# Performance work log

Hardware: AMD Instinct MI355X
Metric: run time of the kernel (lower is better)

Reference implementation:

```python
import jax, jax.numpy as jnp
import numpy as np

B, S, D, H = 2, 2048, 1024, 16
DK = D // H
EPS = 1e-6  # torch RMSNorm default eps=None -> eps = finfo.eps? torch uses eps=None meaning torch.finfo(dtype).eps; use 1.1920929e-07
RMS_EPS = 1.1920929e-07


def setup_inputs() -> dict:
    key = jax.random.key(0)
    ks = jax.random.split(key, 10)
    std = 1.0 / np.sqrt(D)
    inp = {
        "x": jax.random.normal(ks[0], (B, S, D), jnp.float32),
        "mask": jnp.tril(jnp.ones((S, S), jnp.int32))[None, None],  # causal [1,1,S,S]
        "wq": jax.random.uniform(ks[1], (D, D), jnp.float32, -std, std),
        "bq": jax.random.uniform(ks[2], (D,), jnp.float32, -std, std),
        "wk": jax.random.uniform(ks[3], (D, D), jnp.float32, -std, std),
        "bk": jax.random.uniform(ks[4], (D,), jnp.float32, -std, std),
        "wv": jax.random.uniform(ks[5], (D, D), jnp.float32, -std, std),
        "bv": jax.random.uniform(ks[6], (D,), jnp.float32, -std, std),
        "wo": jax.random.uniform(ks[7], (D, D), jnp.float32, -std, std),
        "bo": jax.random.uniform(ks[8], (D,), jnp.float32, -std, std),
        "g": jnp.ones((D,), jnp.float32),  # RMSNorm weight
    }
    return inp


def reference(x, mask, wq, bq, wk, bk, wv, bv, wo, bo, g):
    # pre-RMSNorm
    ms = jnp.mean(x * x, axis=-1, keepdims=True)
    normed = x * jax.lax.rsqrt(ms + RMS_EPS) * g
    # QKV projections (torch Linear: y = x @ W^T + b), split into heads [B,H,S,DK]
    def proj(w, b):
        y = jnp.einsum('bsd,ed->bse', normed, w) + b
        return y.reshape(B, S, H, DK).transpose(0, 2, 1, 3)
    Q, K, V = proj(wq, bq), proj(wk, bk), proj(wv, bv)
    scores = jnp.einsum('bhqd,bhkd->bhqk', Q, K) / jnp.sqrt(jnp.float32(DK))
    scores = jnp.where(mask == 0, jnp.float32(-1e9), scores)
    attn = jax.nn.softmax(scores, axis=-1)
    ctx = jnp.einsum('bhqk,bhkd->bhqd', attn, V)
    ctx = ctx.transpose(0, 2, 1, 3).reshape(B, S, D)
    out = jnp.einsum('bsd,ed->bse', ctx, wo) + bo
    return x + out, attn
```

## Files before the change

### kernel.cpp

```cpp
#include <hip/hip_runtime.h>


typedef unsigned short u16;
typedef __attribute__((ext_vector_type(8))) short bf8_t;
typedef __attribute__((ext_vector_type(4))) float f4_t;

#define S_LEN 2048
#define NHEAD 16
#define RMS_EPS 1.1920929e-07f

__device__ inline u16 f2bf(float f) {
  union { float f; unsigned int i; } v; v.f = f;
  unsigned int r = v.i + 0x7fffu + ((v.i >> 16) & 1u);
  return (u16)(r >> 16);
}

__device__ inline void gll16(const void* g, void* l) {
  __builtin_amdgcn_global_load_lds(
      (const __attribute__((address_space(1))) void*)g,
      (__attribute__((address_space(3))) void*)l, 16, 0, 0);
}

__global__ __launch_bounds__(256) void prep_k(
    const float* __restrict__ wq, const float* __restrict__ wk,
    const float* __restrict__ wv, const float* __restrict__ wo,
    const float* __restrict__ bq, const float* __restrict__ bk,
    const float* __restrict__ bv, u16* __restrict__ Wcat,
    u16* __restrict__ Wob, float* __restrict__ bcat) {
  int idx = blockIdx.x * 256 + threadIdx.x;
  if (idx < 786432) {
    int z = idx / 262144, r = idx - z * 262144;
    const float* s = z == 0 ? wq : z == 1 ? wk : wv;
    float4 v = ((const float4*)s)[r];
    ((ushort4*)Wcat)[idx] =
        make_ushort4(f2bf(v.x), f2bf(v.y), f2bf(v.z), f2bf(v.w));
  } else if (idx < 786432 + 262144) {
    int r = idx - 786432;
    float4 v = ((const float4*)wo)[r];
    ((ushort4*)Wob)[r] = make_ushort4(f2bf(v.x), f2bf(v.y), f2bf(v.z), f2bf(v.w));
  } else if (idx < 786432 + 262144 + 768) {
    int r = idx - (786432 + 262144);
    int z = r >> 8, rr = r & 255;
    const float* s = z == 0 ? bq : z == 1 ? bk : bv;
    ((float4*)bcat)[r] = ((const float4*)s)[rr];
  }
}

__global__ __launch_bounds__(256) void rmsnorm_k(const float* __restrict__ x,
                                                 const float* __restrict__ g,
                                                 u16* __restrict__ out) {
  int row = blockIdx.x, tid = threadIdx.x;
  float4 v = ((const float4*)(x + (size_t)row * 1024))[tid];
  float ss = v.x * v.x + v.y * v.y + v.z * v.z + v.w * v.w;
#pragma unroll
  for (int o = 32; o > 0; o >>= 1) ss += __shfl_xor(ss, o);
  __shared__ float red[4];
  int wid = tid >> 6, lane = tid & 63;
  if (lane == 0) red[wid] = ss;
  __syncthreads();
  float rs = rsqrtf((red[0] + red[1] + red[2] + red[3]) * (1.0f / 1024.0f) +
                    RMS_EPS);
  float4 gv = ((const float4*)g)[tid];
  ((ushort4*)(out + (size_t)row * 1024))[tid] =
      make_ushort4(f2bf(v.x * rs * gv.x), f2bf(v.y * rs * gv.y),
                   f2bf(v.z * rs * gv.z), f2bf(v.w * rs * gv.w));
}

template <int MODE>
__global__ __launch_bounds__(256, 2) void gemm_mfma(
    const u16* __restrict__ A, const u16* __restrict__ Bm,
    const float* __restrict__ bias, const float* __restrict__ resid,
    u16* __restrict__ Oq, u16* __restrict__ Ok, u16* __restrict__ Ov,
    float* __restrict__ out1) {
  __shared__ u16 As[128 * 64];
  __shared__ u16 Bs[128 * 64];
  const int m0 = blockIdx.y * 128, n0 = blockIdx.x * 128;
  const int tid = threadIdx.x, l = tid & 63, w = tid >> 6;
  const int wr = w >> 1, wc = w & 1, lg = l >> 4, lo = l & 15;
  const int arow = tid >> 3;
  const int acol = (tid & 7) * 8;

  f4_t acc[4][4];
#pragma unroll
  for (int i = 0; i < 4; i++)
#pragma unroll
    for (int j = 0; j < 4; j++) acc[i][j] = {0.f, 0.f, 0.f, 0.f};

  for (int k0 = 0; k0 < 1024; k0 += 64) {
#pragma unroll
    for (int r = 0; r < 4; r++) {
      gll16(A + (size_t)(m0 + r * 32 + arow) * 1024 + k0 + acol,
            (char*)As + r * 4096 + w * 1024);
      gll16(Bm + (size_t)(n0 + r * 32 + arow) * 1024 + k0 + acol,
            (char*)Bs + r * 4096 + w * 1024);
    }
    __syncthreads();
#pragma unroll
    for (int ks = 0; ks < 2; ks++) {
      bf8_t af[4], bf[4];
#pragma unroll
      for (int mi = 0; mi < 4; mi++)
        af[mi] = *(const bf8_t*)(As + (wr * 64 + mi * 16 + lo) * 64 + ks * 32 +
                                 lg * 8);
#pragma unroll
      for (int ni = 0; ni < 4; ni++)
        bf[ni] = *(const bf8_t*)(Bs + (wc * 64 + ni * 16 + lo) * 64 + ks * 32 +
                                 lg * 8);
#pragma unroll
      for (int mi = 0; mi < 4; mi++)
#pragma unroll
        for (int ni = 0; ni < 4; ni++)
          acc[mi][ni] = __builtin_amdgcn_mfma_f32_16x16x32_bf16(
              af[mi], bf[ni], acc[mi][ni], 0, 0, 0);
    }
    __syncthreads();
  }

  if (MODE == 0) {
    const int z = n0 >> 10;
    u16* ob = z == 0 ? Oq : z == 1 ? Ok : Ov;
#pragma unroll
    for (int mi = 0; mi < 4; mi++)
#pragma unroll
      for (int ni = 0; ni < 4; ni++)
#pragma unroll
        for (int j = 0; j < 4; j++) {
          int m = m0 + wr * 64 + mi * 16 + lg * 4 + j;
          int n = n0 + wc * 64 + ni * 16 + lo;
          int nn = n & 1023, h = nn >> 6, d = nn & 63;
          int b = m >> 11, s = m & 2047;
          u16 vv = f2bf(acc[mi][ni][j] + bias[n]);
          if (z < 2)
            ob[(((size_t)(b * 16 + h) * 2048 + s) << 6) + d] = vv;
          else
            ob[((size_t)(b * 16 + h) * 64 + d) * 2048 + s] = vv;
        }
  } else {
#pragma unroll
    for (int mi = 0; mi < 4; mi++)
#pragma unroll
      for (int ni = 0; ni < 4; ni++)
#pragma unroll
        for (int j = 0; j < 4; j++) {
          int m = m0 + wr * 64 + mi * 16 + lg * 4 + j;
          int n = n0 + wc * 64 + ni * 16 + lo;
          out1[(size_t)m * 1024 + n] =
              acc[mi][ni][j] + bias[n] + resid[(size_t)m * 1024 + n];
        }
  }
}

__global__ __launch_bounds__(256, 2) void attn_k(
    const u16* __restrict__ Qb, const u16* __restrict__ Kb,
    const u16* __restrict__ Vt, float* __restrict__ attn,
    u16* __restrict__ ctx) {
  const int qt = blockIdx.x, bh = blockIdx.y;
  const int tid = threadIdx.x, l = tid & 63, w = tid >> 6;
  const int wr = w >> 1, wc = w & 1, lg = l >> 4, lo = l & 15;
  const int q0 = qt * 128, nkt = qt + 1;

  __shared__ u16 Pl[128 * 136];
  __shared__ u16 Vs[64 * 136];
  __shared__ float mred[2][128], lred[2][128];

  const u16* Qp = Qb + (size_t)bh * (2048 * 64);
  const u16* Kp = Kb + (size_t)bh * (2048 * 64);
  const u16* Vp = Vt + (size_t)bh * (64 * 2048);
  float* Ap = attn + (size_t)bh * ((size_t)2048 * 2048);

  {
    const int c0 = nkt * 128, cols4 = (2048 - c0) >> 2;
    float4 z4 = make_float4(0.f, 0.f, 0.f, 0.f);
    for (int r = 0; r < 128; r++) {
      float4* rp = (float4*)(Ap + (size_t)(q0 + r) * 2048 + c0);
      for (int c = tid; c < cols4; c += 256) rp[c] = z4;
    }
  }

  bf8_t qf[4][2];
#pragma unroll
  for (int mi = 0; mi < 4; mi++)
#pragma unroll
    for (int ks = 0; ks < 2; ks++)
      qf[mi][ks] = *(const bf8_t*)(Qp +
                                   (size_t)(q0 + wr * 64 + mi * 16 + lo) * 64 +
                                   ks * 32 + lg * 8);

  float rm[4][4], rl[4][4];
#pragma unroll
  for (int mi = 0; mi < 4; mi++)
#pragma unroll
    for (int j = 0; j < 4; j++) { rm[mi][j] = -3.0e38f; rl[mi][j] = 0.f; }

  for (int kt = 0; kt < nkt; kt++) {
    const int k0 = kt * 128;
    f4_t sa[4][4];
#pragma unroll
    for (int i = 0; i < 4; i++)
#pragma unroll
      for (int j = 0; j < 4; j++) sa[i][j] = {0.f, 0.f, 0.f, 0.f};
#pragma unroll
    for (int ks = 0; ks < 2; ks++) {
      bf8_t kf[4];
#pragma unroll
      for (int ni = 0; ni < 4; ni++)
        kf[ni] = *(const bf8_t*)(Kp +
                                 (size_t)(k0 + wc * 64 + ni * 16 + lo) * 64 +
                                 ks * 32 + lg * 8);
#pragma unroll
      for (int mi = 0; mi < 4; mi++)
#pragma unroll
        for (int ni = 0; ni < 4; ni++)
          sa[mi][ni] = __builtin_amdgcn_mfma_f32_16x16x32_bf16(
              qf[mi][ks], kf[ni], sa[mi][ni], 0, 0, 0);
    }
    const bool diag = (kt == qt);
#pragma unroll
    for (int mi = 0; mi < 4; mi++) {
#pragma unroll
      for (int j = 0; j < 4; j++) {
        const int qrow = q0 + wr * 64 + mi * 16 + lg * 4 + j;
        float sv[4], tmax = -3.0e38f;
#pragma unroll
        for (int ni = 0; ni < 4; ni++) {
          float s = sa[mi][ni][j] * 0.125f;
          if (diag && (k0 + wc * 64 + ni * 16 + lo > qrow)) s = -3.0e38f;
          sv[ni] = s;
          tmax = fmaxf(tmax, s);
        }
        tmax = fmaxf(tmax, __shfl_xor(tmax, 1));
        tmax = fmaxf(tmax, __shfl_xor(tmax, 2));
        tmax = fmaxf(tmax, __shfl_xor(tmax, 4));
        tmax = fmaxf(tmax, __shfl_xor(tmax, 8));
        const float nm = fmaxf(rm[mi][j], tmax);
        float ss = 0.f;
#pragma unroll
        for (int ni = 0; ni < 4; ni++) ss += __expf(sv[ni] - nm);
        ss += __shfl_xor(ss, 1);
        ss += __shfl_xor(ss, 2);
        ss += __shfl_xor(ss, 4);
        ss += __shfl_xor(ss, 8);
        rl[mi][j] = rl[mi][j] * __expf(rm[mi][j] - nm) + ss;
        rm[mi][j] = nm;
      }
    }
  }
  if (lo == 0) {
#pragma unroll
    for (int mi = 0; mi < 4; mi++)
#pragma unroll
      for (int j = 0; j < 4; j++) {
        int r = wr * 64 + mi * 16 + lg * 4 + j;
        mred[wc][r] = rm[mi][j];
        lred[wc][r] = rl[mi][j];
      }
  }
  __syncthreads();
#pragma unroll
  for (int mi = 0; mi < 4; mi++)
#pragma unroll
    for (int j = 0; j < 4; j++) {
      int r = wr * 64 + mi * 16 + lg * 4 + j;
      float m1 = mred[0][r], m2 = mred[1][r];
      float M = fmaxf(m1, m2);
      float L = lred[0][r] * __expf(m1 - M) + lred[1][r] * __expf(m2 - M);
      rm[mi][j] = M;
      rl[mi][j] = 1.0f / L;
    }

  f4_t oa[4][2];
#pragma unroll
  for (int i = 0; i < 4; i++)
#pragma unroll
    for (int j = 0; j < 2; j++) oa[i][j] = {0.f, 0.f, 0.f, 0.f};

  for (int kt = 0; kt < nkt; kt++) {
    const int k0 = kt * 128;
    f4_t sa[4][4];
#pragma unroll
    for (int i = 0; i < 4; i++)
#pragma unroll
      for (int j = 0; j < 4; j++) sa[i][j] = {0.f, 0.f, 0.f, 0.f};
#pragma unroll
    for (int ks = 0; ks < 2; ks++) {
      bf8_t kf[4];
#pragma unroll
      for (int ni = 0; ni < 4; ni++)
        kf[ni] = *(const bf8_t*)(Kp +
                                 (size_t)(k0 + wc * 64 + ni * 16 + lo) * 64 +
                                 ks * 32 + lg * 8);
#pragma unroll
      for (int mi = 0; mi < 4; mi++)
#pragma unroll
        for (int ni = 0; ni < 4; ni++)
          sa[mi][ni] = __builtin_amdgcn_mfma_f32_16x16x32_bf16(
              qf[mi][ks], kf[ni], sa[mi][ni], 0, 0, 0);
    }
#pragma unroll
    for (int it = 0; it < 4; it++) {
      int gr = it * 256 + tid, d = gr >> 4, gcol = gr & 15;
      *(int4*)(&Vs[d * 136 + gcol * 8]) =
          *(const int4*)(Vp + (size_t)d * 2048 + k0 + gcol * 8);
    }
    const bool diag = (kt == qt);
#pragma unroll
    for (int mi = 0; mi < 4; mi++) {
#pragma unroll
      for (int j = 0; j < 4; j++) {
        const int qrow = q0 + wr * 64 + mi * 16 + lg * 4 + j;
        const int qloc = wr * 64 + mi * 16 + lg * 4 + j;
        float* arow = Ap + (size_t)qrow * 2048 + k0 + wc * 64;
#pragma unroll
        for (int ni = 0; ni < 4; ni++) {
          float s = sa[mi][ni][j] * 0.125f;
          float p = __expf(s - rm[mi][j]) * rl[mi][j];
          if (diag && (k0 + wc * 64 + ni * 16 + lo > qrow)) p = 0.f;
          arow[ni * 16 + lo] = p;
          Pl[qloc * 136 + wc * 64 + ni * 16 + lo] = f2bf(p);
        }
      }
    }
    __syncthreads();
#pragma unroll
    for (int ks = 0; ks < 4; ks++) {
      bf8_t pf[4], vf[2];
#pragma unroll
      for (int mi = 0; mi < 4; mi++)
        pf[mi] =
            *(const bf8_t*)(&Pl[(wr * 64 + mi * 16 + lo) * 136 + ks * 32 +
                                lg * 8]);
#pragma unroll
      for (int ni = 0; ni < 2; ni++)
        vf[ni] =
            *(const bf8_t*)(&Vs[(wc * 32 + ni * 16 + lo) * 136 + ks * 32 +
                                lg * 8]);
#pragma unroll
      for (int mi = 0; mi < 4; mi++)
#pragma unroll
        for (int ni = 0; ni < 2; ni++)
          oa[mi][ni] = __builtin_amdgcn_mfma_f32_16x16x32_bf16(
              pf[mi], vf[ni], oa[mi][ni], 0, 0, 0);
    }
    __syncthreads();
  }

  const int b = bh >> 4, h = bh & 15;
#pragma unroll
  for (int mi = 0; mi < 4; mi++)
#pragma unroll
    for (int ni = 0; ni < 2; ni++)
#pragma unroll
      for (int j = 0; j < 4; j++) {
        int q = q0 + wr * 64 + mi * 16 + lg * 4 + j;
        int d = wc * 32 + ni * 16 + lo;
        ctx[(size_t)(b * 2048 + q) * 1024 + h * 64 + d] = f2bf(oa[mi][ni][j]);
      }
}

extern "C" void kernel_launch(void* const* d_in, const int* in_sizes, int n_in,
                              void* d_out, int out_size, void* d_ws,
                              size_t ws_size, hipStream_t stream) {
  const float* x = (const float*)d_in[0];
  const float* wq = (const float*)d_in[2];
  const float* bq = (const float*)d_in[3];
  const float* wk = (const float*)d_in[4];
  const float* bk = (const float*)d_in[5];
  const float* wv = (const float*)d_in[6];
  const float* bv = (const float*)d_in[7];
  const float* wo = (const float*)d_in[8];
  const float* bo = (const float*)d_in[9];
  const float* g = (const float*)d_in[10];

  float* out0 = (float*)d_out;
  float* attn = out0 + (size_t)4096 * 1024;

  u16* nrm = (u16*)d_ws;
  u16* Wcat = nrm + (size_t)4096 * 1024;
  u16* Wob = Wcat + (size_t)3072 * 1024;
  u16* Qbb = Wob + (size_t)1024 * 1024;
  u16* Kbb = Qbb + (size_t)4194304;
  u16* Vtb = Kbb + (size_t)4194304;
  u16* ctxb = Vtb + (size_t)4194304;
  float* bcat = (float*)(ctxb + (size_t)4194304);

  prep_k<<<4099, 256, 0, stream>>>(wq, wk, wv, wo, bq, bk, bv, Wcat, Wob, bcat);
  rmsnorm_k<<<4096, 256, 0, stream>>>(x, g, nrm);
  gemm_mfma<0><<<dim3(24, 32), 256, 0, stream>>>(nrm, Wcat, bcat, nullptr, Qbb,
                                                 Kbb, Vtb, nullptr);
  attn_k<<<dim3(16, 32), 256, 0, stream>>>(Qbb, Kbb, Vtb, attn, ctxb);
  gemm_mfma<1><<<dim3(8, 32), 256, 0, stream>>>(ctxb, Wob, bo, x, nullptr,
                                                nullptr, nullptr, out0);
}
```

Before: 823.1 us.

## Use 8 waves per attention block, fold scale into Q, balance causal tiles

```diff
diff --git a/kernel.cpp b/kernel.cpp
--- a/kernel.cpp
+++ b/kernel.cpp
@@ -119,6 +119,7 @@
   if (MODE == 0) {
     const int z = n0 >> 10;
     u16* ob = z == 0 ? Oq : z == 1 ? Ok : Ov;
+    const float sc = (z == 0) ? 0.125f : 1.0f;
 #pragma unroll
     for (int mi = 0; mi < 4; mi++)
 #pragma unroll
@@ -129,7 +130,7 @@
           int n = n0 + wc * 64 + ni * 16 + lo;
           int nn = n & 1023, h = nn >> 6, d = nn & 63;
           int b = m >> 11, s = m & 2047;
-          u16 vv = f2bf(acc[mi][ni][j] + bias[n]);
+          u16 vv = f2bf((acc[mi][ni][j] + bias[n]) * sc);
           if (z < 2)
             ob[(((size_t)(b * 16 + h) * 2048 + s) << 6) + d] = vv;
           else
@@ -150,18 +151,19 @@
   }
 }
 
-__global__ __launch_bounds__(256, 2) void attn_k(
+__global__ __launch_bounds__(512, 4) void attn_k(
     const u16* __restrict__ Qb, const u16* __restrict__ Kb,
     const u16* __restrict__ Vt, float* __restrict__ attn,
     u16* __restrict__ ctx) {
-  const int qt = blockIdx.x, bh = blockIdx.y;
+  const int bh = blockIdx.y;
+  const int qt = (bh < 16) ? blockIdx.x : 15 - blockIdx.x;
   const int tid = threadIdx.x, l = tid & 63, w = tid >> 6;
-  const int wr = w >> 1, wc = w & 1, lg = l >> 4, lo = l & 15;
+  const int wr = w >> 2, wc = w & 3, lg = l >> 4, lo = l & 15;
   const int q0 = qt * 128, nkt = qt + 1;
 
   __shared__ u16 Pl[128 * 136];
   __shared__ u16 Vs[64 * 136];
-  __shared__ float mred[2][128], lred[2][128];
+  __shared__ float mred[4][128], lred[4][128];
 
   const u16* Qp = Qb + (size_t)bh * (2048 * 64);
   const u16* Kp = Kb + (size_t)bh * (2048 * 64);
@@ -173,7 +175,7 @@
     float4 z4 = make_float4(0.f, 0.f, 0.f, 0.f);
     for (int r = 0; r < 128; r++) {
       float4* rp = (float4*)(Ap + (size_t)(q0 + r) * 2048 + c0);
-      for (int c = tid; c < cols4; c += 256) rp[c] = z4;
+      for (int c = tid; c < cols4; c += 512) rp[c] = z4;
     }
   }
 
@@ -194,23 +196,23 @@
 
   for (int kt = 0; kt < nkt; kt++) {
     const int k0 = kt * 128;
-    f4_t sa[4][4];
+    f4_t sa[4][2];
 #pragma unroll
     for (int i = 0; i < 4; i++)
 #pragma unroll
-      for (int j = 0; j < 4; j++) sa[i][j] = {0.f, 0.f, 0.f, 0.f};
+      for (int j = 0; j < 2; j++) sa[i][j] = {0.f, 0.f, 0.f, 0.f};
 #pragma unroll
     for (int ks = 0; ks < 2; ks++) {
-      bf8_t kf[4];
-#pragma unroll
-      for (int ni = 0; ni < 4; ni++)
+      bf8_t kf[2];
+#pragma unroll
+      for (int ni = 0; ni < 2; ni++)
         kf[ni] = *(const bf8_t*)(Kp +
-                                 (size_t)(k0 + wc * 64 + ni * 16 + lo) * 64 +
+                                 (size_t)(k0 + wc * 32 + ni * 16 + lo) * 64 +
                                  ks * 32 + lg * 8);
 #pragma unroll
       for (int mi = 0; mi < 4; mi++)
 #pragma unroll
-        for (int ni = 0; ni < 4; ni++)
+        for (int ni = 0; ni < 2; ni++)
           sa[mi][ni] = __builtin_amdgcn_mfma_f32_16x16x32_bf16(
               qf[mi][ks], kf[ni], sa[mi][ni], 0, 0, 0);
     }
@@ -220,11 +222,11 @@
 #pragma unroll
       for (int j = 0; j < 4; j++) {
         const int qrow = q0 + wr * 64 + mi * 16 + lg * 4 + j;
-        float sv[4], tmax = -3.0e38f;
-#pragma unroll
-        for (int ni = 0; ni < 4; ni++) {
-          float s = sa[mi][ni][j] * 0.125f;
-          if (diag && (k0 + wc * 64 + ni * 16 + lo > qrow)) s = -3.0e38f;
+        float sv[2], tmax = -3.0e38f;
+#pragma unroll
+        for (int ni = 0; ni < 2; ni++) {
+          float s = sa[mi][ni][j];
+          if (diag && (k0 + wc * 32 + ni * 16 + lo > qrow)) s = -3.0e38f;
           sv[ni] = s;
           tmax = fmaxf(tmax, s);
         }
@@ -233,9 +235,7 @@
         tmax = fmaxf(tmax, __shfl_xor(tmax, 4));
         tmax = fmaxf(tmax, __shfl_xor(tmax, 8));
         const float nm = fmaxf(rm[mi][j], tmax);
-        float ss = 0.f;
-#pragma unroll
-        for (int ni = 0; ni < 4; ni++) ss += __expf(sv[ni] - nm);
+        float ss = __expf(sv[0] - nm) + __expf(sv[1] - nm);
         ss += __shfl_xor(ss, 1);
         ss += __shfl_xor(ss, 2);
         ss += __shfl_xor(ss, 4);
@@ -261,44 +261,45 @@
 #pragma unroll
     for (int j = 0; j < 4; j++) {
       int r = wr * 64 + mi * 16 + lg * 4 + j;
-      float m1 = mred[0][r], m2 = mred[1][r];
-      float M = fmaxf(m1, m2);
-      float L = lred[0][r] * __expf(m1 - M) + lred[1][r] * __expf(m2 - M);
+      float M = fmaxf(fmaxf(mred[0][r], mred[1][r]),
+                      fmaxf(mred[2][r], mred[3][r]));
+      float L = lred[0][r] * __expf(mred[0][r] - M) +
+                lred[1][r] * __expf(mred[1][r] - M) +
+                lred[2][r] * __expf(mred[2][r] - M) +
+                lred[3][r] * __expf(mred[3][r] - M);
       rm[mi][j] = M;
       rl[mi][j] = 1.0f / L;
     }
 
-  f4_t oa[4][2];
-#pragma unroll
-  for (int i = 0; i < 4; i++)
-#pragma unroll
-    for (int j = 0; j < 2; j++) oa[i][j] = {0.f, 0.f, 0.f, 0.f};
+  f4_t oa[4];
+#pragma unroll
+  for (int i = 0; i < 4; i++) oa[i] = {0.f, 0.f, 0.f, 0.f};
 
   for (int kt = 0; kt < nkt; kt++) {
     const int k0 = kt * 128;
-    f4_t sa[4][4];
+    f4_t sa[4][2];
 #pragma unroll
     for (int i = 0; i < 4; i++)
 #pragma unroll
-      for (int j = 0; j < 4; j++) sa[i][j] = {0.f, 0.f, 0.f, 0.f};
+      for (int j = 0; j < 2; j++) sa[i][j] = {0.f, 0.f, 0.f, 0.f};
 #pragma unroll
     for (int ks = 0; ks < 2; ks++) {
-      bf8_t kf[4];
-#pragma unroll
-      for (int ni = 0; ni < 4; ni++)
+      bf8_t kf[2];
+#pragma unroll
+      for (int ni = 0; ni < 2; ni++)
         kf[ni] = *(const bf8_t*)(Kp +
-                                 (size_t)(k0 + wc * 64 + ni * 16 + lo) * 64 +
+                                 (size_t)(k0 + wc * 32 + ni * 16 + lo) * 64 +
                                  ks * 32 + lg * 8);
 #pragma unroll
       for (int mi = 0; mi < 4; mi++)
 #pragma unroll
-        for (int ni = 0; ni < 4; ni++)
+        for (int ni = 0; ni < 2; ni++)
           sa[mi][ni] = __builtin_amdgcn_mfma_f32_16x16x32_bf16(
               qf[mi][ks], kf[ni], sa[mi][ni], 0, 0, 0);
     }
 #pragma unroll
-    for (int it = 0; it < 4; it++) {
-      int gr = it * 256 + tid, d = gr >> 4, gcol = gr & 15;
+    for (int it = 0; it < 2; it++) {
+      int gr = it * 512 + tid, d = gr >> 4, gcol = gr & 15;
       *(int4*)(&Vs[d * 136 + gcol * 8]) =
           *(const int4*)(Vp + (size_t)d * 2048 + k0 + gcol * 8);
     }
@@ -309,37 +310,30 @@
       for (int j = 0; j < 4; j++) {
         const int qrow = q0 + wr * 64 + mi * 16 + lg * 4 + j;
         const int qloc = wr * 64 + mi * 16 + lg * 4 + j;
-        float* arow = Ap + (size_t)qrow * 2048 + k0 + wc * 64;
-#pragma unroll
-        for (int ni = 0; ni < 4; ni++) {
-          float s = sa[mi][ni][j] * 0.125f;
-          float p = __expf(s - rm[mi][j]) * rl[mi][j];
-          if (diag && (k0 + wc * 64 + ni * 16 + lo > qrow)) p = 0.f;
+        float* arow = Ap + (size_t)qrow * 2048 + k0 + wc * 32;
+#pragma unroll
+        for (int ni = 0; ni < 2; ni++) {
+          float p = __expf(sa[mi][ni][j] - rm[mi][j]) * rl[mi][j];
+          if (diag && (k0 + wc * 32 + ni * 16 + lo > qrow)) p = 0.f;
           arow[ni * 16 + lo] = p;
-          Pl[qloc * 136 + wc * 64 + ni * 16 + lo] = f2bf(p);
+          Pl[qloc * 136 + wc * 32 + ni * 16 + lo] = f2bf(p);
         }
       }
     }
     __syncthreads();
 #pragma unroll
     for (int ks = 0; ks < 4; ks++) {
-      bf8_t pf[4], vf[2];
+      bf8_t pf[4], vf;
 #pragma unroll
       for (int mi = 0; mi < 4; mi++)
         pf[mi] =
             *(const bf8_t*)(&Pl[(wr * 64 + mi * 16 + lo) * 136 + ks * 32 +
                                 lg * 8]);
-#pragma unroll
-      for (int ni = 0; ni < 2; ni++)
-        vf[ni] =
-            *(const bf8_t*)(&Vs[(wc * 32 + ni * 16 + lo) * 136 + ks * 32 +
-                                lg * 8]);
-#pragma unroll
-      for (int mi = 0; mi < 4; mi++)
-#pragma unroll
-        for (int ni = 0; ni < 2; ni++)
-          oa[mi][ni] = __builtin_amdgcn_mfma_f32_16x16x32_bf16(
-              pf[mi], vf[ni], oa[mi][ni], 0, 0, 0);
+      vf = *(const bf8_t*)(&Vs[(wc * 16 + lo) * 136 + ks * 32 + lg * 8]);
+#pragma unroll
+      for (int mi = 0; mi < 4; mi++)
+        oa[mi] = __builtin_amdgcn_mfma_f32_16x16x32_bf16(pf[mi], vf, oa[mi],
+                                                         0, 0, 0);
     }
     __syncthreads();
   }
@@ -348,13 +342,11 @@
 #pragma unroll
   for (int mi = 0; mi < 4; mi++)
 #pragma unroll
-    for (int ni = 0; ni < 2; ni++)
-#pragma unroll
-      for (int j = 0; j < 4; j++) {
-        int q = q0 + wr * 64 + mi * 16 + lg * 4 + j;
-        int d = wc * 32 + ni * 16 + lo;
-        ctx[(size_t)(b * 2048 + q) * 1024 + h * 64 + d] = f2bf(oa[mi][ni][j]);
-      }
+    for (int j = 0; j < 4; j++) {
+      int q = q0 + wr * 64 + mi * 16 + lg * 4 + j;
+      int d = wc * 16 + lo;
+      ctx[(size_t)(b * 2048 + q) * 1024 + h * 64 + d] = f2bf(oa[mi][j]);
+    }
 }
 
 extern "C" void kernel_launch(void* const* d_in, const int* in_sizes, int n_in,
@@ -387,7 +379,7 @@
   rmsnorm_k<<<4096, 256, 0, stream>>>(x, g, nrm);
   gemm_mfma<0><<<dim3(24, 32), 256, 0, stream>>>(nrm, Wcat, bcat, nullptr, Qbb,
                                                  Kbb, Vtb, nullptr);
-  attn_k<<<dim3(16, 32), 256, 0, stream>>>(Qbb, Kbb, Vtb, attn, ctxb);
+  attn_k<<<dim3(16, 32), 512, 0, stream>>>(Qbb, Kbb, Vtb, attn, ctxb);
   gemm_mfma<1><<<dim3(8, 32), 256, 0, stream>>>(ctxb, Wob, bo, x, nullptr,
                                                 nullptr, nullptr, out0);
 }
```

New measurement: 916.6 us. 1.11x slower.
